# Optimization experiments

Measured on AMD Instinct MI355X. Metric: run time of the kernel, lower is better.

The kernel has to match this reference:

```python
import jax, jax.numpy as jnp
import numpy as np

NUM_HEADS = 12
H_PATCH = 14
W_PATCH = 14
ROPE_BASE = 10000.0


def _rope_2d(head_dim):
    # 2D RoPE: first half of head_dim encodes row (h), second half encodes col (w).
    half = head_dim // 2
    inv_freq = 1.0 / (ROPE_BASE ** (jnp.arange(0, half, 2, dtype=jnp.float32) / half))  # [half/2]
    ys = jnp.arange(H_PATCH)
    xs = jnp.arange(W_PATCH)
    yy, xx = jnp.meshgrid(ys, xs, indexing='ij')
    h_idx = yy.reshape(-1).astype(jnp.float32)  # [N]
    w_idx = xx.reshape(-1).astype(jnp.float32)  # [N]
    freqs_h = h_idx[:, None] * inv_freq[None, :]  # [N, half/2]
    freqs_w = w_idx[:, None] * inv_freq[None, :]  # [N, half/2]
    emb = jnp.concatenate([freqs_h, freqs_w], axis=-1)  # [N, half]
    emb = jnp.concatenate([emb, emb], axis=-1)          # [N, head_dim]
    return jnp.cos(emb), jnp.sin(emb)


def _rotate_half(x):
    d = x.shape[-1] // 2
    return jnp.concatenate([-x[..., d:], x[..., :d]], axis=-1)


def reference(x, qkv_w, qkv_b, proj_w, proj_b):
    BxT, N, C = x.shape
    hd = C // NUM_HEADS
    qkv = x @ qkv_w.T + qkv_b                                    # [BxT, N, 3C]
    qkv = qkv.reshape(BxT, N, 3, NUM_HEADS, hd)
    qkv = jnp.transpose(qkv, (2, 0, 3, 1, 4))                    # [3, BxT, H, N, hd]
    q, k, v = qkv[0], qkv[1], qkv[2]
    cos, sin = _rope_2d(hd)                                      # [N, hd]
    cos = cos[None, None, :, :]
    sin = sin[None, None, :, :]
    q = q * cos + _rotate_half(q) * sin
    k = k * cos + _rotate_half(k) * sin
    scale = hd ** -0.5
    attn = jnp.einsum('bhqd,bhkd->bhqk', q, k) * scale           # [BxT, H, N, N]
    attn = jax.nn.softmax(attn, axis=-1)
    out = jnp.einsum('bhqk,bhkd->bhqd', attn, v)                 # [BxT, H, N, hd]
    out = jnp.transpose(out, (0, 2, 1, 3)).reshape(BxT, N, C)
    out = out @ proj_w.T + proj_b
    return out


def setup_inputs() -> dict:
    key = jax.random.key(0)
    ks = jax.random.split(key, 5)
    C = 768
    return {
        'x': jax.random.normal(ks[0], (128, 196, C), dtype=jnp.float32),
        'qkv_w': jax.random.normal(ks[1], (3 * C, C), dtype=jnp.float32) * (C ** -0.5),
        'qkv_b': jax.random.normal(ks[2], (3 * C,), dtype=jnp.float32) * 0.02,
        'proj_w': jax.random.normal(ks[3], (C, C), dtype=jnp.float32) * (C ** -0.5),
        'proj_b': jax.random.normal(ks[4], (C,), dtype=jnp.float32) * 0.02,
    }
```

## Files before the change

### kernel.cpp

```cpp
#include <hip/hip_runtime.h>
#include <hip/hip_bf16.h>

typedef __attribute__((ext_vector_type(8))) short short8;
typedef __attribute__((ext_vector_type(4))) float f32x4;

#define GLD16(gp, lp) \
  __builtin_amdgcn_global_load_lds((const __attribute__((address_space(1))) void*)(gp), \
                                   (__attribute__((address_space(3))) void*)(lp), 16, 0, 0)

__device__ __forceinline__ f32x4 mfma_bf16(short8 a, short8 b, f32x4 c) {
  return __builtin_amdgcn_mfma_f32_16x16x32_bf16(a, b, c, 0, 0, 0);
}

__global__ __launch_bounds__(256) void cast_bf16_kernel(const float* __restrict__ src,
                                                        __hip_bfloat16* __restrict__ dst,
                                                        int n4) {
  int i = blockIdx.x * 256 + threadIdx.x;
  if (i >= n4) return;
  float4 v = reinterpret_cast<const float4*>(src)[i];
  ushort4 o;
  o.x = __builtin_bit_cast(unsigned short, __float2bfloat16(v.x));
  o.y = __builtin_bit_cast(unsigned short, __float2bfloat16(v.y));
  o.z = __builtin_bit_cast(unsigned short, __float2bfloat16(v.z));
  o.w = __builtin_bit_cast(unsigned short, __float2bfloat16(v.w));
  reinterpret_cast<ushort4*>(dst)[i] = o;
}

__global__ __launch_bounds__(256) void rope_table_kernel(float* __restrict__ cosT,
                                                         float* __restrict__ sinT) {
  int i = blockIdx.x * 256 + threadIdx.x;
  if (i >= 196 * 64) return;
  int t = i >> 6, d = i & 63;
  int c = d & 31;
  float pos = (c < 16) ? (float)(t / 14) : (float)(t % 14);
  int j = c & 15;
  float invf = expf(-(float)j * 0.5756462732485114f);
  float ang = pos * invf;
  cosT[i] = cosf(ang);
  sinT[i] = sinf(ang);
}

__global__ __launch_bounds__(256) void gemm_qkv_kernel(
    const __hip_bfloat16* __restrict__ A, const __hip_bfloat16* __restrict__ W,
    const float* __restrict__ bias, const float* __restrict__ cosT,
    const float* __restrict__ sinT, __hip_bfloat16* __restrict__ qb,
    __hip_bfloat16* __restrict__ kb, __hip_bfloat16* __restrict__ vb) {
  __shared__ __align__(16) __hip_bfloat16 As[128 * 64];
  __shared__ __align__(16) __hip_bfloat16 Bs[128 * 64];
  const int tid = threadIdx.x;
  const int id = blockIdx.x;
  const int sup = id / 72, rem = id % 72;
  const int bm = sup * 4 + rem / 18;
  const int bn = rem % 18;
  const int lane = tid & 63, wv = tid >> 6;
  const int wm = wv >> 1, wn = wv & 1;
  const int quad = lane >> 4, ln = lane & 15;

  const int r0 = tid >> 3;
  const int csw = ((tid & 7) ^ (r0 & 7)) * 8;
  const __hip_bfloat16* Ag = A + ((long)(bm * 128 + r0) * 768 + csw);
  const __hip_bfloat16* Wg = W + ((long)(bn * 128 + r0) * 768 + csw);
  __hip_bfloat16* As0 = As + tid * 8;
  __hip_bfloat16* Bs0 = Bs + tid * 8;

  const int c0 = (quad ^ (ln & 7)) * 8;
  const int c1 = c0 ^ 32;

  f32x4 acc[4][4];
#pragma unroll
  for (int i = 0; i < 4; i++)
#pragma unroll
    for (int j = 0; j < 4; j++) acc[i][j] = (f32x4){0.f, 0.f, 0.f, 0.f};

  for (int k0 = 0; k0 < 768; k0 += 64) {
    GLD16(Ag + k0,            As0);
    GLD16(Ag + 32 * 768 + k0, As0 + 2048);
    GLD16(Ag + 64 * 768 + k0, As0 + 4096);
    GLD16(Ag + 96 * 768 + k0, As0 + 6144);
    GLD16(Wg + k0,            Bs0);
    GLD16(Wg + 32 * 768 + k0, Bs0 + 2048);
    GLD16(Wg + 64 * 768 + k0, Bs0 + 4096);
    GLD16(Wg + 96 * 768 + k0, Bs0 + 6144);
    __syncthreads();
#pragma unroll
    for (int kk = 0; kk < 2; kk++) {
      const int cc = kk ? c1 : c0;
      short8 af[4], bf[4];
#pragma unroll
      for (int i = 0; i < 4; i++)
        af[i] = *(const short8*)(As + (wm * 64 + i * 16 + ln) * 64 + cc);
#pragma unroll
      for (int j = 0; j < 4; j++)
        bf[j] = *(const short8*)(Bs + (wn * 64 + j * 16 + ln) * 64 + cc);
#pragma unroll
      for (int i = 0; i < 4; i++)
#pragma unroll
        for (int j = 0; j < 4; j++) acc[i][j] = mfma_bf16(af[i], bf[j], acc[i][j]);
    }
    __syncthreads();
  }

  const int ncolbase = bn * 128 + wn * 64;
  const int s = ncolbase / 768;
  const int hh = (ncolbase % 768) >> 6;
  __hip_bfloat16* outb = (s == 0) ? qb : ((s == 1) ? kb : vb);
  float bi[4];
#pragma unroll
  for (int j = 0; j < 4; j++) bi[j] = bias[ncolbase + j * 16 + ln];
  const bool dorope = (s < 2);

#pragma unroll
  for (int i = 0; i < 4; i++) {
#pragma unroll
    for (int r = 0; r < 4; r++) {
      int m = bm * 128 + wm * 64 + i * 16 + quad * 4 + r;
      int b = m / 196, t = m - b * 196;
      float v0 = acc[i][0][r] + bi[0];
      float v1 = acc[i][1][r] + bi[1];
      float v2 = acc[i][2][r] + bi[2];
      float v3 = acc[i][3][r] + bi[3];
      if (dorope) {
        const float* ct = cosT + t * 64 + ln;
        const float* st = sinT + t * 64 + ln;
        float c0f = ct[0], c1f = ct[16], c2f = ct[32], c3f = ct[48];
        float s0 = st[0], s1 = st[16], s2 = st[32], s3 = st[48];
        float w0 = v0 * c0f - v2 * s0;
        float w1 = v1 * c1f - v3 * s1;
        float w2 = v2 * c2f + v0 * s2;
        float w3 = v3 * c3f + v1 * s3;
        v0 = w0; v1 = w1; v2 = w2; v3 = w3;
      }
      __hip_bfloat16* op = outb + ((long)(b * 12 + hh) * 196 + t) * 64 + ln;
      op[0]  = __float2bfloat16(v0);
      op[16] = __float2bfloat16(v1);
      op[32] = __float2bfloat16(v2);
      op[48] = __float2bfloat16(v3);
    }
  }
}

__global__ __launch_bounds__(256) void attn_kernel(
    const __hip_bfloat16* __restrict__ qb, const __hip_bfloat16* __restrict__ kb,
    const __hip_bfloat16* __restrict__ vb, __hip_bfloat16* __restrict__ att) {
  __shared__ __align__(16) __hip_bfloat16 Vt[64 * 232];
  __shared__ __align__(16) __hip_bfloat16 Ps[4][16 * 232];
  const int bh = blockIdx.x;
  const int b = bh / 12, h = bh - b * 12;
  const int tid = threadIdx.x;
  const int lane = tid & 63, wv = tid >> 6;
  const int quad = lane >> 4, ln = lane & 15;
  const __hip_bfloat16* qg = qb + (long)bh * (196 * 64);
  const __hip_bfloat16* kg = kb + (long)bh * (196 * 64);
  const __hip_bfloat16* vg = vb + (long)bh * (196 * 64);

  for (int ch = tid; ch < 224 * 8; ch += 256) {
    int row = ch >> 3, c = (ch & 7) * 8;
    unsigned short vals[8] = {0, 0, 0, 0, 0, 0, 0, 0};
    if (row < 196) *(uint4*)vals = *(const uint4*)(vg + row * 64 + c);
#pragma unroll
    for (int u = 0; u < 8; u++)
      ((unsigned short*)Vt)[(c + u) * 232 + row] = vals[u];
  }

  __hip_bfloat16* Pw = &Ps[wv][0];
#pragma unroll
  for (int r = 0; r < 4; r++)
    Pw[(quad * 4 + r) * 232 + 208 + ln] = __float2bfloat16(0.f);
  __syncthreads();

  for (int qt = wv; qt < 13; qt += 4) {
    int tok = qt * 16 + ln;
    if (tok > 195) tok = 195;
    short8 aq0 = *(const short8*)(qg + tok * 64 + quad * 8);
    short8 aq1 = *(const short8*)(qg + tok * 64 + 32 + quad * 8);

    f32x4 sacc[13];
#pragma unroll
    for (int ct = 0; ct < 13; ct++) {
      int krow = ct * 16 + ln;
      if (krow > 195) krow = 195;
      const __hip_bfloat16* kp = kg + krow * 64 + quad * 8;
      short8 b0 = *(const short8*)kp;
      short8 b1 = *(const short8*)(kp + 32);
      f32x4 cacc = (f32x4){0.f, 0.f, 0.f, 0.f};
      cacc = mfma_bf16(aq0, b0, cacc);
      cacc = mfma_bf16(aq1, b1, cacc);
      sacc[ct] = cacc;
    }

    float sm[4] = {0.f, 0.f, 0.f, 0.f};
#pragma unroll
    for (int ct = 0; ct < 13; ct++) {
      bool valid = (ct * 16 + ln) < 196;
#pragma unroll
      for (int r = 0; r < 4; r++) {
        float p = valid ? __expf(sacc[ct][r] * 0.125f) : 0.f;
        sm[r] += p;
        Pw[(quad * 4 + r) * 232 + ct * 16 + ln] = __float2bfloat16(p);
      }
    }
#pragma unroll
    for (int mk = 1; mk < 16; mk <<= 1) {
#pragma unroll
      for (int r = 0; r < 4; r++) sm[r] += __shfl_xor(sm[r], mk, 64);
    }
    asm volatile("" ::: "memory");

    f32x4 o[4];
#pragma unroll
    for (int j = 0; j < 4; j++) o[j] = (f32x4){0.f, 0.f, 0.f, 0.f};
#pragma unroll
    for (int kt = 0; kt < 7; kt++) {
      short8 pa = *(const short8*)(Pw + ln * 232 + kt * 32 + quad * 8);
#pragma unroll
      for (int j = 0; j < 4; j++) {
        short8 bv = *(const short8*)(Vt + (j * 16 + ln) * 232 + kt * 32 + quad * 8);
        o[j] = mfma_bf16(pa, bv, o[j]);
      }
    }
    asm volatile("" ::: "memory");

    float rl[4];
#pragma unroll
    for (int r = 0; r < 4; r++) rl[r] = 1.0f / sm[r];
    int trow = qt * 16 + quad * 4;
#pragma unroll
    for (int r = 0; r < 4; r++) {
      int t = trow + r;
      if (t < 196) {
        __hip_bfloat16* op = att + (long)(b * 196 + t) * 768 + h * 64 + ln;
#pragma unroll
        for (int j = 0; j < 4; j++) op[j * 16] = __float2bfloat16(o[j][r] * rl[r]);
      }
    }
  }
}

__global__ __launch_bounds__(256) void gemm_proj_kernel(
    const __hip_bfloat16* __restrict__ A, const __hip_bfloat16* __restrict__ W,
    const float* __restrict__ bias, float* __restrict__ out) {
  __shared__ __align__(16) __hip_bfloat16 As[128 * 64];
  __shared__ __align__(16) __hip_bfloat16 Bs[128 * 64];
  const int tid = threadIdx.x;
  const int id = blockIdx.x;
  const int sup = id / 24, rem = id % 24;
  const int bm = sup * 4 + rem / 6;
  const int bn = rem % 6;
  const int lane = tid & 63, wv = tid >> 6;
  const int wm = wv >> 1, wn = wv & 1;
  const int quad = lane >> 4, ln = lane & 15;

  const int r0 = tid >> 3;
  const int csw = ((tid & 7) ^ (r0 & 7)) * 8;
  const __hip_bfloat16* Ag = A + ((long)(bm * 128 + r0) * 768 + csw);
  const __hip_bfloat16* Wg = W + ((long)(bn * 128 + r0) * 768 + csw);
  __hip_bfloat16* As0 = As + tid * 8;
  __hip_bfloat16* Bs0 = Bs + tid * 8;

  const int c0 = (quad ^ (ln & 7)) * 8;
  const int c1 = c0 ^ 32;

  f32x4 acc[4][4];
#pragma unroll
  for (int i = 0; i < 4; i++)
#pragma unroll
    for (int j = 0; j < 4; j++) acc[i][j] = (f32x4){0.f, 0.f, 0.f, 0.f};

  for (int k0 = 0; k0 < 768; k0 += 64) {
    GLD16(Ag + k0,            As0);
    GLD16(Ag + 32 * 768 + k0, As0 + 2048);
    GLD16(Ag + 64 * 768 + k0, As0 + 4096);
    GLD16(Ag + 96 * 768 + k0, As0 + 6144);
    GLD16(Wg + k0,            Bs0);
    GLD16(Wg + 32 * 768 + k0, Bs0 + 2048);
    GLD16(Wg + 64 * 768 + k0, Bs0 + 4096);
    GLD16(Wg + 96 * 768 + k0, Bs0 + 6144);
    __syncthreads();
#pragma unroll
    for (int kk = 0; kk < 2; kk++) {
      const int cc = kk ? c1 : c0;
      short8 af[4], bf[4];
#pragma unroll
      for (int i = 0; i < 4; i++)
        af[i] = *(const short8*)(As + (wm * 64 + i * 16 + ln) * 64 + cc);
#pragma unroll
      for (int j = 0; j < 4; j++)
        bf[j] = *(const short8*)(Bs + (wn * 64 + j * 16 + ln) * 64 + cc);
#pragma unroll
      for (int i = 0; i < 4; i++)
#pragma unroll
        for (int j = 0; j < 4; j++) acc[i][j] = mfma_bf16(af[i], bf[j], acc[i][j]);
    }
    __syncthreads();
  }

  const int ncolbase = bn * 128 + wn * 64;
  float bi[4];
#pragma unroll
  for (int j = 0; j < 4; j++) bi[j] = bias[ncolbase + j * 16 + ln];
#pragma unroll
  for (int i = 0; i < 4; i++) {
#pragma unroll
    for (int r = 0; r < 4; r++) {
      int m = bm * 128 + wm * 64 + i * 16 + quad * 4 + r;
      float* op = out + (long)m * 768 + ncolbase + ln;
      op[0]  = acc[i][0][r] + bi[0];
      op[16] = acc[i][1][r] + bi[1];
      op[32] = acc[i][2][r] + bi[2];
      op[48] = acc[i][3][r] + bi[3];
    }
  }
}

extern "C" void kernel_launch(void* const* d_in, const int* in_sizes, int n_in,
                              void* d_out, int out_size, void* d_ws, size_t ws_size,
                              hipStream_t stream) {
  const float* x      = (const float*)d_in[0];
  const float* qkv_w  = (const float*)d_in[1];
  const float* qkv_b  = (const float*)d_in[2];
  const float* proj_w = (const float*)d_in[3];
  const float* proj_b = (const float*)d_in[4];
  float* out = (float*)d_out;
  (void)in_sizes; (void)n_in; (void)out_size; (void)ws_size;

  char* ws = (char*)d_ws;
  size_t off = 0;
  auto alloc = [&](size_t bytes) -> void* {
    void* p = (void*)(ws + off);
    off += (bytes + 255) & ~(size_t)255;
    return p;
  };
  const size_t MB0 = (size_t)25088 * 768 * 2;
  __hip_bfloat16* xb   = (__hip_bfloat16*)alloc(MB0);
  __hip_bfloat16* w1b  = (__hip_bfloat16*)alloc((size_t)2304 * 768 * 2);
  __hip_bfloat16* w2b  = (__hip_bfloat16*)alloc((size_t)768 * 768 * 2);
  float* cosT          = (float*)alloc(196 * 64 * 4);
  float* sinT          = (float*)alloc(196 * 64 * 4);
  __hip_bfloat16* qbuf = (__hip_bfloat16*)alloc(MB0);
  __hip_bfloat16* kbuf = (__hip_bfloat16*)alloc(MB0);
  __hip_bfloat16* vbuf = (__hip_bfloat16*)alloc(MB0);
  __hip_bfloat16* attb = xb;

  cast_bf16_kernel<<<18816, 256, 0, stream>>>(x, xb, 25088 * 768 / 4);
  cast_bf16_kernel<<<1728, 256, 0, stream>>>(qkv_w, w1b, 2304 * 768 / 4);
  cast_bf16_kernel<<<576, 256, 0, stream>>>(proj_w, w2b, 768 * 768 / 4);
  rope_table_kernel<<<49, 256, 0, stream>>>(cosT, sinT);
  gemm_qkv_kernel<<<3528, 256, 0, stream>>>(xb, w1b, qkv_b, cosT, sinT,
                                            qbuf, kbuf, vbuf);
  attn_kernel<<<1536, 256, 0, stream>>>(qbuf, kbuf, vbuf, attb);
  gemm_proj_kernel<<<1176, 256, 0, stream>>>(attb, w2b, proj_b, out);
}
```

Before: 380.8 us.

## Rewrite QKV GEMM as 256x256 double-buffered 8-wave pipelined kernel

```diff
diff --git a/kernel.cpp b/kernel.cpp
--- a/kernel.cpp
+++ b/kernel.cpp
@@ -10,6 +10,12 @@
 
 __device__ __forceinline__ f32x4 mfma_bf16(short8 a, short8 b, f32x4 c) {
   return __builtin_amdgcn_mfma_f32_16x16x32_bf16(a, b, c, 0, 0, 0);
+}
+
+__device__ __forceinline__ void bar() {
+  asm volatile("" ::: "memory");
+  __builtin_amdgcn_s_barrier();
+  asm volatile("" ::: "memory");
 }
 
 __global__ __launch_bounds__(256) void cast_bf16_kernel(const float* __restrict__ src,
@@ -40,67 +46,153 @@
   sinT[i] = sinf(ang);
 }
 
-__global__ __launch_bounds__(256) void gemm_qkv_kernel(
+__global__ __launch_bounds__(512, 2) void gemm_qkv_kernel(
     const __hip_bfloat16* __restrict__ A, const __hip_bfloat16* __restrict__ W,
     const float* __restrict__ bias, const float* __restrict__ cosT,
     const float* __restrict__ sinT, __hip_bfloat16* __restrict__ qb,
     __hip_bfloat16* __restrict__ kb, __hip_bfloat16* __restrict__ vb) {
-  __shared__ __align__(16) __hip_bfloat16 As[128 * 64];
-  __shared__ __align__(16) __hip_bfloat16 Bs[128 * 64];
+  __shared__ __align__(16) __hip_bfloat16 As[2][256 * 64];
+  __shared__ __align__(16) __hip_bfloat16 Bs[2][256 * 64];
   const int tid = threadIdx.x;
   const int id = blockIdx.x;
-  const int sup = id / 72, rem = id % 72;
-  const int bm = sup * 4 + rem / 18;
-  const int bn = rem % 18;
+  const int bm = id / 9, bn = id % 9;
   const int lane = tid & 63, wv = tid >> 6;
-  const int wm = wv >> 1, wn = wv & 1;
+  const int wm = wv >> 2, wn = wv & 3;
   const int quad = lane >> 4, ln = lane & 15;
 
   const int r0 = tid >> 3;
   const int csw = ((tid & 7) ^ (r0 & 7)) * 8;
-  const __hip_bfloat16* Ag = A + ((long)(bm * 128 + r0) * 768 + csw);
-  const __hip_bfloat16* Wg = W + ((long)(bn * 128 + r0) * 768 + csw);
-  __hip_bfloat16* As0 = As + tid * 8;
-  __hip_bfloat16* Bs0 = Bs + tid * 8;
-
-  const int c0 = (quad ^ (ln & 7)) * 8;
-  const int c1 = c0 ^ 32;
-
-  f32x4 acc[4][4];
-#pragma unroll
-  for (int i = 0; i < 4; i++)
+  const __hip_bfloat16* Ag = A + ((long)(bm * 256 + r0) * 768 + csw);
+  const __hip_bfloat16* Wg = W + ((long)(bn * 256 + r0) * 768 + csw);
+
+#define STG_A(BB, HH, KT) do { \
+    GLD16(Ag + (long)((HH) * 128) * 768 + (KT) * 64,      &As[BB][(HH) * 8192] + tid * 8); \
+    GLD16(Ag + (long)((HH) * 128 + 64) * 768 + (KT) * 64, &As[BB][(HH) * 8192 + 4096] + tid * 8); \
+  } while (0)
+#define STG_B(BB, HH, KT) do { \
+    GLD16(Wg + (long)((HH) * 128) * 768 + (KT) * 64,      &Bs[BB][(HH) * 8192] + tid * 8); \
+    GLD16(Wg + (long)((HH) * 128 + 64) * 768 + (KT) * 64, &Bs[BB][(HH) * 8192 + 4096] + tid * 8); \
+  } while (0)
+
+  const int aoff0 = (wm * 128 + ln) * 64;
+  const int boff0 = (wn * 64 + ln) * 64;
+  const int ch0 = ((0 + quad) ^ (ln & 7)) * 8;
+  const int ch1 = ((4 + quad) ^ (ln & 7)) * 8;
+
+  f32x4 acc[8][4];
+#pragma unroll
+  for (int i = 0; i < 8; i++)
 #pragma unroll
     for (int j = 0; j < 4; j++) acc[i][j] = (f32x4){0.f, 0.f, 0.f, 0.f};
 
-  for (int k0 = 0; k0 < 768; k0 += 64) {
-    GLD16(Ag + k0,            As0);
-    GLD16(Ag + 32 * 768 + k0, As0 + 2048);
-    GLD16(Ag + 64 * 768 + k0, As0 + 4096);
-    GLD16(Ag + 96 * 768 + k0, As0 + 6144);
-    GLD16(Wg + k0,            Bs0);
-    GLD16(Wg + 32 * 768 + k0, Bs0 + 2048);
-    GLD16(Wg + 64 * 768 + k0, Bs0 + 4096);
-    GLD16(Wg + 96 * 768 + k0, Bs0 + 6144);
-    __syncthreads();
-#pragma unroll
-    for (int kk = 0; kk < 2; kk++) {
-      const int cc = kk ? c1 : c0;
-      short8 af[4], bf[4];
-#pragma unroll
-      for (int i = 0; i < 4; i++)
-        af[i] = *(const short8*)(As + (wm * 64 + i * 16 + ln) * 64 + cc);
-#pragma unroll
-      for (int j = 0; j < 4; j++)
-        bf[j] = *(const short8*)(Bs + (wn * 64 + j * 16 + ln) * 64 + cc);
-#pragma unroll
-      for (int i = 0; i < 4; i++)
-#pragma unroll
-        for (int j = 0; j < 4; j++) acc[i][j] = mfma_bf16(af[i], bf[j], acc[i][j]);
-    }
-    __syncthreads();
-  }
-
-  const int ncolbase = bn * 128 + wn * 64;
+  STG_B(0, 0, 0); STG_B(0, 1, 0); STG_A(0, 0, 0); STG_A(0, 1, 0);
+  STG_B(1, 0, 1); STG_B(1, 1, 1); STG_A(1, 0, 1);
+  asm volatile("s_waitcnt vmcnt(6)" ::: "memory");
+  bar();
+
+  short8 bf[4][2], a0[4][2], a1[4][2];
+
+#define MFMA_Q(AF, FB, GB) \
+  _Pragma("unroll") \
+  for (int f = 0; f < 4; f++) { \
+    _Pragma("unroll") \
+    for (int g = 0; g < 2; g++) { \
+      acc[(FB) + f][(GB) + g] = mfma_bf16(AF[f][0], bf[(GB) + g][0], acc[(FB) + f][(GB) + g]); \
+      acc[(FB) + f][(GB) + g] = mfma_bf16(AF[f][1], bf[(GB) + g][1], acc[(FB) + f][(GB) + g]); \
+    } \
+  }
+
+#pragma unroll 1
+  for (int t = 0; t < 6; ++t) {
+    const int more = (t < 5);
+    const int ktO = 2 * t + 1, ktN = 2 * t + 2, ktN1 = 2 * t + 3;
+#pragma unroll
+    for (int g = 0; g < 4; g++) {
+      bf[g][0] = *(const short8*)(&Bs[0][boff0 + g * 1024 + ch0]);
+      bf[g][1] = *(const short8*)(&Bs[0][boff0 + g * 1024 + ch1]);
+    }
+#pragma unroll
+    for (int f = 0; f < 4; f++) {
+      a0[f][0] = *(const short8*)(&As[0][aoff0 + f * 1024 + ch0]);
+      a0[f][1] = *(const short8*)(&As[0][aoff0 + f * 1024 + ch1]);
+    }
+    STG_A(1, 1, ktO);
+    bar();
+    __builtin_amdgcn_s_setprio(1);
+    MFMA_Q(a0, 0, 0)
+    __builtin_amdgcn_s_setprio(0);
+    bar();
+#pragma unroll
+    for (int f = 0; f < 4; f++) {
+      a1[f][0] = *(const short8*)(&As[0][aoff0 + 4096 + f * 1024 + ch0]);
+      a1[f][1] = *(const short8*)(&As[0][aoff0 + 4096 + f * 1024 + ch1]);
+    }
+    if (more) STG_B(0, 0, ktN);
+    bar();
+    __builtin_amdgcn_s_setprio(1);
+    MFMA_Q(a1, 4, 0)
+    __builtin_amdgcn_s_setprio(0);
+    bar();
+    if (more) STG_B(0, 1, ktN);
+    bar();
+    __builtin_amdgcn_s_setprio(1);
+    MFMA_Q(a1, 4, 2)
+    __builtin_amdgcn_s_setprio(0);
+    bar();
+    if (more) STG_A(0, 0, ktN);
+    bar();
+    __builtin_amdgcn_s_setprio(1);
+    MFMA_Q(a0, 0, 2)
+    __builtin_amdgcn_s_setprio(0);
+    if (more) { asm volatile("s_waitcnt vmcnt(6)" ::: "memory"); }
+    else      { asm volatile("s_waitcnt vmcnt(0)" ::: "memory"); }
+    bar();
+#pragma unroll
+    for (int g = 0; g < 4; g++) {
+      bf[g][0] = *(const short8*)(&Bs[1][boff0 + g * 1024 + ch0]);
+      bf[g][1] = *(const short8*)(&Bs[1][boff0 + g * 1024 + ch1]);
+    }
+#pragma unroll
+    for (int f = 0; f < 4; f++) {
+      a0[f][0] = *(const short8*)(&As[1][aoff0 + f * 1024 + ch0]);
+      a0[f][1] = *(const short8*)(&As[1][aoff0 + f * 1024 + ch1]);
+    }
+    if (more) STG_A(0, 1, ktN);
+    bar();
+    __builtin_amdgcn_s_setprio(1);
+    MFMA_Q(a0, 0, 0)
+    __builtin_amdgcn_s_setprio(0);
+    bar();
+#pragma unroll
+    for (int f = 0; f < 4; f++) {
+      a1[f][0] = *(const short8*)(&As[1][aoff0 + 4096 + f * 1024 + ch0]);
+      a1[f][1] = *(const short8*)(&As[1][aoff0 + 4096 + f * 1024 + ch1]);
+    }
+    if (more) STG_B(1, 0, ktN1);
+    bar();
+    __builtin_amdgcn_s_setprio(1);
+    MFMA_Q(a1, 4, 0)
+    __builtin_amdgcn_s_setprio(0);
+    bar();
+    if (more) STG_B(1, 1, ktN1);
+    bar();
+    __builtin_amdgcn_s_setprio(1);
+    MFMA_Q(a1, 4, 2)
+    __builtin_amdgcn_s_setprio(0);
+    bar();
+    if (more) STG_A(1, 0, ktN1);
+    bar();
+    __builtin_amdgcn_s_setprio(1);
+    MFMA_Q(a0, 0, 2)
+    __builtin_amdgcn_s_setprio(0);
+    if (more) { asm volatile("s_waitcnt vmcnt(6)" ::: "memory"); }
+    bar();
+  }
+#undef MFMA_Q
+#undef STG_A
+#undef STG_B
+
+  const int ncolbase = bn * 256 + wn * 64;
   const int s = ncolbase / 768;
   const int hh = (ncolbase % 768) >> 6;
   __hip_bfloat16* outb = (s == 0) ? qb : ((s == 1) ? kb : vb);
@@ -110,18 +202,18 @@
   const bool dorope = (s < 2);
 
 #pragma unroll
-  for (int i = 0; i < 4; i++) {
+  for (int f = 0; f < 8; f++) {
 #pragma unroll
     for (int r = 0; r < 4; r++) {
-      int m = bm * 128 + wm * 64 + i * 16 + quad * 4 + r;
-      int b = m / 196, t = m - b * 196;
-      float v0 = acc[i][0][r] + bi[0];
-      float v1 = acc[i][1][r] + bi[1];
-      float v2 = acc[i][2][r] + bi[2];
-      float v3 = acc[i][3][r] + bi[3];
+      int m = bm * 256 + wm * 128 + f * 16 + quad * 4 + r;
+      int bb = m / 196, tt = m - bb * 196;
+      float v0 = acc[f][0][r] + bi[0];
+      float v1 = acc[f][1][r] + bi[1];
+      float v2 = acc[f][2][r] + bi[2];
+      float v3 = acc[f][3][r] + bi[3];
       if (dorope) {
-        const float* ct = cosT + t * 64 + ln;
-        const float* st = sinT + t * 64 + ln;
+        const float* ct = cosT + tt * 64 + ln;
+        const float* st = sinT + tt * 64 + ln;
         float c0f = ct[0], c1f = ct[16], c2f = ct[32], c3f = ct[48];
         float s0 = st[0], s1 = st[16], s2 = st[32], s3 = st[48];
         float w0 = v0 * c0f - v2 * s0;
@@ -130,7 +222,7 @@
         float w3 = v3 * c3f + v1 * s3;
         v0 = w0; v1 = w1; v2 = w2; v3 = w3;
       }
-      __hip_bfloat16* op = outb + ((long)(b * 12 + hh) * 196 + t) * 64 + ln;
+      __hip_bfloat16* op = outb + ((long)(bb * 12 + hh) * 196 + tt) * 64 + ln;
       op[0]  = __float2bfloat16(v0);
       op[16] = __float2bfloat16(v1);
       op[32] = __float2bfloat16(v2);
@@ -345,8 +437,8 @@
   cast_bf16_kernel<<<1728, 256, 0, stream>>>(qkv_w, w1b, 2304 * 768 / 4);
   cast_bf16_kernel<<<576, 256, 0, stream>>>(proj_w, w2b, 768 * 768 / 4);
   rope_table_kernel<<<49, 256, 0, stream>>>(cosT, sinT);
-  gemm_qkv_kernel<<<3528, 256, 0, stream>>>(xb, w1b, qkv_b, cosT, sinT,
-                                            qbuf, kbuf, vbuf);
+  gemm_qkv_kernel<<<882, 512, 0, stream>>>(xb, w1b, qkv_b, cosT, sinT,
+                                           qbuf, kbuf, vbuf);
   attn_kernel<<<1536, 256, 0, stream>>>(qbuf, kbuf, vbuf, attb);
   gemm_proj_kernel<<<1176, 256, 0, stream>>>(attb, w2b, proj_b, out);
 }
```

Result: no change. 382.8 us (+0.5%).
